# Optimization experiments

Measured on AMD Instinct MI355X. Metric: run time of the kernel, lower is better.

## Reference

```python
import jax, jax.numpy as jnp
import numpy as np

B, D, NF, L, G = 8192, 4096, 16, 32, 64  # batch, input_dim, num_factors, latent_per_factor, num groups
K = D // G  # group size (contiguous equal-size partition of columns)


def setup_inputs() -> dict:
    key = jax.random.key(0)
    k0, k1, k2, k3 = jax.random.split(key, 4)
    x = jax.random.normal(k0, (B, D), dtype=jnp.float32)
    # encoder: Linear(D,128) -> ReLU -> Linear(128, NF*L)
    W1 = jax.random.normal(k1, (D, 128), dtype=jnp.float32) * 0.02
    b1 = jnp.zeros((128,), dtype=jnp.float32)
    W2 = jax.random.normal(k2, (128, NF * L), dtype=jnp.float32) * 0.02
    b2 = jnp.zeros((NF * L,), dtype=jnp.float32)
    # k_matrix decoders: one [K, L] matrix per group, stacked -> [G, K, L]
    decoders = jax.random.normal(k3, (G, K, L), dtype=jnp.float32)
    return {"x": x, "W1": W1, "b1": b1, "W2": W2, "b2": b2, "decoders": decoders}


def reference(x, W1, b1, W2, b2, decoders):
    # encoder
    z = jax.nn.relu(x @ W1 + b1) @ W2 + b2                 # [B, NF*L]
    # reconstructions[:, group_g] = sum_j z_j @ D_g^T  ==  (sum_j z_j) @ D_g^T
    z_sum = z.reshape(x.shape[0], NF, L).sum(axis=1)        # [B, L]
    recon = jnp.einsum('bl,gkl->bgk', z_sum, decoders)      # [B, G, K]
    recon = recon.reshape(x.shape[0], G * K)                # [B, D] (contiguous groups)
    return (z, recon)
```

## Files before the change

### kernel.cpp

```cpp
#include <hip/hip_runtime.h>
#include <hip/hip_bf16.h>

#define BATCH 8192
#define DIN   4096
#define H1    128
#define NLAT  512
#define LAT   32
#define BM    16
#define BK    128
#define NSTEP (DIN / BK)
#define APITCH 136

typedef short bf16x8 __attribute__((ext_vector_type(8)));
typedef float f32x4  __attribute__((ext_vector_type(4)));

static __device__ __forceinline__ unsigned short f2bf(float f) {
  union { float f; unsigned u; } v; v.f = f;
  return (unsigned short)((v.u + 0x7FFFu + ((v.u >> 16) & 1u)) >> 16);
}

static __device__ __forceinline__ void cvtw8(unsigned short* p, f32x4 a, f32x4 b) {
  union { bf16x8 v; unsigned short u[8]; } o;
#pragma unroll
  for (int j = 0; j < 4; j++) { o.u[j] = f2bf(a[j]); o.u[4 + j] = f2bf(b[j]); }
  *(bf16x8*)p = o.v;
}

__global__ void prep_all(const float* __restrict__ W1, const float* __restrict__ W2,
                         const float* __restrict__ dec,
                         unsigned short* __restrict__ W1B,
                         unsigned short* __restrict__ W2B,
                         float* __restrict__ decT) {
  int b = blockIdx.x;
  int t = threadIdx.x;
  if (b < 256) {
    int gi = (b << 2) + (t >> 6);
    int lane = t & 63;
    int kb = ((gi >> 3) << 5) + ((lane >> 4) << 3);
    int c = ((gi & 7) << 4) + (lane & 15);
    union { bf16x8 v; unsigned short u[8]; } o;
#pragma unroll
    for (int j = 0; j < 8; j++) o.u[j] = f2bf(W1[(size_t)(kb + j) * H1 + c]);
    *(bf16x8*)(W1B + (((size_t)gi << 6) + (lane & 63)) * 8) = o.v;
  } else if (b < 288) {
    int gi = ((b - 256) << 2) + (t >> 6);
    int lane = t & 63;
    int kb = ((gi >> 5) << 5) + ((lane >> 4) << 3);
    int c = ((gi & 31) << 4) + (lane & 15);
    union { bf16x8 v; unsigned short u[8]; } o;
#pragma unroll
    for (int j = 0; j < 8; j++) o.u[j] = f2bf(W2[(size_t)(kb + j) * NLAT + c]);
    *(bf16x8*)(W2B + (((size_t)gi << 6) + lane) * 8) = o.v;
  } else {
    __shared__ float tbuf[32][33];
    int d0 = (b - 288) * 32;
    int tx = t & 31, ty = t >> 5;
#pragma unroll
    for (int i = 0; i < 32; i += 8)
      tbuf[ty + i][tx] = dec[(size_t)(d0 + ty + i) * LAT + tx];
    __syncthreads();
#pragma unroll
    for (int i = 0; i < 32; i += 8)
      decT[(size_t)(ty + i) * DIN + (d0 + tx)] = tbuf[tx][ty + i];
  }
}

__global__ __launch_bounds__(256, 4) void enc_kernel(
    const float* __restrict__ x, const unsigned short* __restrict__ W1B,
    const unsigned short* __restrict__ W2B,
    const float* __restrict__ b1, const float* __restrict__ b2,
    float* __restrict__ zout, float* __restrict__ zsumg) {
  __shared__ unsigned short As[2][BM * APITCH];
  __shared__ unsigned short hs[BM * APITCH];
  __shared__ float zsp[4][BM][33];

  const int t = threadIdx.x;
  const int rbase = blockIdx.x << 4;
  const int w = t >> 6, lane = t & 63;
  const int g = lane >> 4, fr = lane & 15;

  const int srow = t >> 4, skq = (t & 15) << 3;
  const float* xp = x + (size_t)(rbase + srow) * DIN + skq;
  const int wofs = srow * APITCH + skq;

  f32x4 acc[2];
  acc[0] = (f32x4){0.f, 0.f, 0.f, 0.f};
  acc[1] = (f32x4){0.f, 0.f, 0.f, 0.f};

  cvtw8(&As[0][wofs], *(const f32x4*)xp, *(const f32x4*)(xp + 4));
  __syncthreads();

  for (int s = 0; s < NSTEP; ++s) {
    f32x4 ra0, ra1;
    const bool more = (s + 1) < NSTEP;
    if (more) {
      ra0 = *(const f32x4*)(xp + (s + 1) * BK);
      ra1 = *(const f32x4*)(xp + (s + 1) * BK + 4);
    }
    const unsigned short* ab = &As[s & 1][0];
#pragma unroll
    for (int k32 = 0; k32 < 4; ++k32) {
      bf16x8 a0 = *(const bf16x8*)(ab + fr * APITCH + (((k32 << 2) + g) << 3));
#pragma unroll
      for (int cc = 0; cc < 2; ++cc) {
        bf16x8 bv = *(const bf16x8*)(W1B +
            ((((size_t)(((s << 2) + k32) << 3)) + (w << 1) + cc) << 9) + (lane << 3));
        acc[cc] = __builtin_amdgcn_mfma_f32_16x16x32_bf16(a0, bv, acc[cc], 0, 0, 0);
      }
    }
    if (more)
      cvtw8(&As[(s + 1) & 1][wofs], ra0, ra1);
    __syncthreads();
  }

  {
#pragma unroll
    for (int cc = 0; cc < 2; ++cc) {
      const int col = (w << 5) + (cc << 4) + fr;
      const float b1v = b1[col];
#pragma unroll
      for (int j = 0; j < 4; j++) {
        float h = fmaxf(acc[cc][j] + b1v, 0.f);
        hs[((g << 2) + j) * APITCH + col] = f2bf(h);
      }
    }
  }
  __syncthreads();

  f32x4 acc2[8];
#pragma unroll
  for (int i = 0; i < 8; i++) acc2[i] = (f32x4){0.f, 0.f, 0.f, 0.f};
#pragma unroll
  for (int k32 = 0; k32 < 4; ++k32) {
    bf16x8 a0 = *(const bf16x8*)(hs + fr * APITCH + (((k32 << 2) + g) << 3));
#pragma unroll
    for (int cc = 0; cc < 8; ++cc) {
      bf16x8 bv = *(const bf16x8*)(W2B +
          (((size_t)((k32 << 5) + (w << 3) + cc)) << 9) + (lane << 3));
      acc2[cc] = __builtin_amdgcn_mfma_f32_16x16x32_bf16(a0, bv, acc2[cc], 0, 0, 0);
    }
  }

  {
    f32x4 zv[8];
#pragma unroll
    for (int cc = 0; cc < 8; ++cc) {
      const float b2v = b2[(w << 7) + (cc << 4) + fr];
#pragma unroll
      for (int j = 0; j < 4; j++) zv[cc][j] = acc2[cc][j] + b2v;
    }
    const int row0 = g << 2;
#pragma unroll
    for (int j = 0; j < 4; j++) {
#pragma unroll
      for (int cc = 0; cc < 8; ++cc)
        zout[(size_t)(rbase + row0 + j) * NLAT + (w << 7) + (cc << 4) + fr] = zv[cc][j];
      zsp[w][row0 + j][fr]      = zv[0][j] + zv[2][j] + zv[4][j] + zv[6][j];
      zsp[w][row0 + j][16 + fr] = zv[1][j] + zv[3][j] + zv[5][j] + zv[7][j];
    }
  }
  __syncthreads();
#pragma unroll
  for (int i = 0; i < 2; i++) {
    int idx = t + (i << 8);
    int r = idx >> 5, l = idx & 31;
    float s = zsp[0][r][l] + zsp[1][r][l] + zsp[2][r][l] + zsp[3][r][l];
    zsumg[(size_t)(rbase + r) * LAT + l] = s;
  }
}

__global__ __launch_bounds__(256) void recon_kernel(
    const float* __restrict__ zsumg, const float* __restrict__ decT,
    float* __restrict__ rout) {
  __shared__ float zs[32][32];
  int t = threadIdx.x;
  int rbase = (blockIdx.x >> 4) << 5;
  int dcol0 = (blockIdx.x & 15) << 8;
  {
    int r = t >> 3, c4 = (t & 7) << 2;
    *(f32x4*)&zs[r][c4] = *(const f32x4*)(zsumg + (size_t)(rbase + r) * LAT + c4);
  }
  __syncthreads();
  int wq = t >> 6, lane = t & 63;
  int r0 = wq << 3;
  int dcol = dcol0 + (lane << 2);
  f32x4 acc[8];
#pragma unroll
  for (int r = 0; r < 8; r++) acc[r] = (f32x4){0.f, 0.f, 0.f, 0.f};
#pragma unroll 4
  for (int l = 0; l < 32; l++) {
    f32x4 dv = *(const f32x4*)(decT + (size_t)l * DIN + dcol);
#pragma unroll
    for (int r = 0; r < 8; r++) {
      float zv = zs[r0 + r][l];
#pragma unroll
      for (int j = 0; j < 4; j++) acc[r][j] += zv * dv[j];
    }
  }
#pragma unroll
  for (int r = 0; r < 8; r++)
    *(f32x4*)(rout + (size_t)(rbase + r0 + r) * DIN + dcol) = acc[r];
}

extern "C" void kernel_launch(void* const* d_in, const int* in_sizes, int n_in,
                              void* d_out, int out_size, void* d_ws, size_t ws_size,
                              hipStream_t stream) {
  const float* x   = (const float*)d_in[0];
  const float* W1  = (const float*)d_in[1];
  const float* b1  = (const float*)d_in[2];
  const float* W2  = (const float*)d_in[3];
  const float* b2  = (const float*)d_in[4];
  const float* dec = (const float*)d_in[5];
  float* zout = (float*)d_out;
  float* rout = zout + (size_t)BATCH * NLAT;

  char* ws = (char*)d_ws;
  unsigned short* W1B = (unsigned short*)ws;
  unsigned short* W2B = (unsigned short*)(ws + (1u << 20));
  float* decT  = (float*)(ws + (1u << 20) + (1u << 17));
  float* zsumg = (float*)(ws + (1u << 20) + (1u << 17) + (1u << 19));

  prep_all<<<dim3(416), 256, 0, stream>>>(W1, W2, dec, W1B, W2B, decT);
  enc_kernel<<<dim3(BATCH / BM), 256, 0, stream>>>(x, W1B, W2B, b1, b2, zout, zsumg);
  recon_kernel<<<dim3(4096), 256, 0, stream>>>(zsumg, decT, rout);
}
```

Before: 90.93 us.

## Split encoder K across warps with private LDS buffers and LDS reduction

The first encoder GEMM now splits the 4096-long K dimension into four slices, one per wavefront. Each wave streams its slice into a private double-buffered, XOR-swizzled LDS tile and computes all 128 hidden columns, so the block-wide barrier inside the K loop goes away. The four partial sums are then reduced through LDS, the bias and ReLU are applied, and the hidden layer is written to a swizzled bf16 tile for the second GEMM. In exchange the kernel uses more LDS and registers, launch bounds drop from 4 to 2 blocks per CU, and there is an extra reduction pass.

```diff
diff --git a/kernel.cpp b/kernel.cpp
--- a/kernel.cpp
+++ b/kernel.cpp
@@ -7,9 +7,9 @@
 #define NLAT  512
 #define LAT   32
 #define BM    16
-#define BK    128
-#define NSTEP (DIN / BK)
-#define APITCH 136
+#define BKW   64
+#define WSTEPS 16
+#define ABUF  1024
 
 typedef short bf16x8 __attribute__((ext_vector_type(8)));
 typedef float f32x4  __attribute__((ext_vector_type(4)));
@@ -41,7 +41,7 @@
     union { bf16x8 v; unsigned short u[8]; } o;
 #pragma unroll
     for (int j = 0; j < 8; j++) o.u[j] = f2bf(W1[(size_t)(kb + j) * H1 + c]);
-    *(bf16x8*)(W1B + (((size_t)gi << 6) + (lane & 63)) * 8) = o.v;
+    *(bf16x8*)(W1B + (((size_t)gi << 6) + lane) * 8) = o.v;
   } else if (b < 288) {
     int gi = ((b - 256) << 2) + (t >> 6);
     int lane = t & 63;
@@ -65,65 +65,94 @@
   }
 }
 
-__global__ __launch_bounds__(256, 4) void enc_kernel(
+__global__ __launch_bounds__(256, 2) void enc_kernel(
     const float* __restrict__ x, const unsigned short* __restrict__ W1B,
     const unsigned short* __restrict__ W2B,
     const float* __restrict__ b1, const float* __restrict__ b2,
     float* __restrict__ zout, float* __restrict__ zsumg) {
-  __shared__ unsigned short As[2][BM * APITCH];
-  __shared__ unsigned short hs[BM * APITCH];
-  __shared__ float zsp[4][BM][33];
+  __shared__ unsigned short Apriv[4 * 2 * ABUF];
+  __shared__ unsigned short hs[16 * 128];
+  __shared__ float pacc[4][16][132];
+  __shared__ float zsp[4][16][33];
 
   const int t = threadIdx.x;
   const int rbase = blockIdx.x << 4;
   const int w = t >> 6, lane = t & 63;
   const int g = lane >> 4, fr = lane & 15;
 
-  const int srow = t >> 4, skq = (t & 15) << 3;
-  const float* xp = x + (size_t)(rbase + srow) * DIN + skq;
-  const int wofs = srow * APITCH + skq;
-
-  f32x4 acc[2];
-  acc[0] = (f32x4){0.f, 0.f, 0.f, 0.f};
-  acc[1] = (f32x4){0.f, 0.f, 0.f, 0.f};
-
-  cvtw8(&As[0][wofs], *(const f32x4*)xp, *(const f32x4*)(xp + 4));
-  __syncthreads();
-
-  for (int s = 0; s < NSTEP; ++s) {
-    f32x4 ra0, ra1;
-    const bool more = (s + 1) < NSTEP;
+  const int srow = lane >> 2, sq = lane & 3;
+  const int k0 = w << 10;
+  const float* xp = x + (size_t)(rbase + srow) * DIN + k0 + (sq << 4);
+  unsigned short* abase = Apriv + (w << 11);
+  const int wg0 = ((sq << 1) ^ (srow & 7)) << 3;
+  const int wg1 = (((sq << 1) | 1) ^ (srow & 7)) << 3;
+  unsigned short* wrow = abase + srow * 64;
+
+  f32x4 acc[8];
+#pragma unroll
+  for (int i = 0; i < 8; i++) acc[i] = (f32x4){0.f, 0.f, 0.f, 0.f};
+
+  {
+    f32x4 q0 = *(const f32x4*)xp;
+    f32x4 q1 = *(const f32x4*)(xp + 4);
+    f32x4 q2 = *(const f32x4*)(xp + 8);
+    f32x4 q3 = *(const f32x4*)(xp + 12);
+    cvtw8(wrow + wg0, q0, q1);
+    cvtw8(wrow + wg1, q2, q3);
+  }
+
+  for (int s = 0; s < WSTEPS; ++s) {
+    f32x4 q0, q1, q2, q3;
+    const bool more = (s + 1) < WSTEPS;
     if (more) {
-      ra0 = *(const f32x4*)(xp + (s + 1) * BK);
-      ra1 = *(const f32x4*)(xp + (s + 1) * BK + 4);
-    }
-    const unsigned short* ab = &As[s & 1][0];
-#pragma unroll
-    for (int k32 = 0; k32 < 4; ++k32) {
-      bf16x8 a0 = *(const bf16x8*)(ab + fr * APITCH + (((k32 << 2) + g) << 3));
-#pragma unroll
-      for (int cc = 0; cc < 2; ++cc) {
-        bf16x8 bv = *(const bf16x8*)(W1B +
-            ((((size_t)(((s << 2) + k32) << 3)) + (w << 1) + cc) << 9) + (lane << 3));
-        acc[cc] = __builtin_amdgcn_mfma_f32_16x16x32_bf16(a0, bv, acc[cc], 0, 0, 0);
+      const float* np = xp + (s + 1) * BKW;
+      q0 = *(const f32x4*)np;
+      q1 = *(const f32x4*)(np + 4);
+      q2 = *(const f32x4*)(np + 8);
+      q3 = *(const f32x4*)(np + 12);
+    }
+    const unsigned short* ab = abase + (s & 1) * ABUF;
+    const int kbase = (w << 5) + (s << 1);
+#pragma unroll
+    for (int k32l = 0; k32l < 2; ++k32l) {
+      bf16x8 a = *(const bf16x8*)(ab + fr * 64 +
+                   ((((k32l << 2) + g) ^ (fr & 7)) << 3));
+      const unsigned short* bp = W1B + (((size_t)(kbase + k32l) << 3) << 9) + (lane << 3);
+#pragma unroll
+      for (int cf = 0; cf < 8; ++cf) {
+        bf16x8 bv = *(const bf16x8*)(bp + ((size_t)cf << 9));
+        acc[cf] = __builtin_amdgcn_mfma_f32_16x16x32_bf16(a, bv, acc[cf], 0, 0, 0);
       }
     }
-    if (more)
-      cvtw8(&As[(s + 1) & 1][wofs], ra0, ra1);
-    __syncthreads();
-  }
-
-  {
-#pragma unroll
-    for (int cc = 0; cc < 2; ++cc) {
-      const int col = (w << 5) + (cc << 4) + fr;
-      const float b1v = b1[col];
-#pragma unroll
-      for (int j = 0; j < 4; j++) {
-        float h = fmaxf(acc[cc][j] + b1v, 0.f);
-        hs[((g << 2) + j) * APITCH + col] = f2bf(h);
-      }
-    }
+    if (more) {
+      unsigned short* wr = abase + ((s + 1) & 1) * ABUF + srow * 64;
+      cvtw8(wr + wg0, q0, q1);
+      cvtw8(wr + wg1, q2, q3);
+    }
+  }
+
+#pragma unroll
+  for (int cf = 0; cf < 8; ++cf)
+#pragma unroll
+    for (int j = 0; j < 4; ++j)
+      pacc[w][(g << 2) + j][(cf << 4) + fr] = acc[cf][j];
+  __syncthreads();
+
+  {
+    const int r = t >> 4, c8 = (t & 15) << 3;
+    f32x4 s0, s1;
+#pragma unroll
+    for (int j = 0; j < 4; j++) { s0[j] = b1[c8 + j]; s1[j] = b1[c8 + 4 + j]; }
+#pragma unroll
+    for (int wv = 0; wv < 4; ++wv) {
+      f32x4 p0 = *(const f32x4*)&pacc[wv][r][c8];
+      f32x4 p1 = *(const f32x4*)&pacc[wv][r][c8 + 4];
+#pragma unroll
+      for (int j = 0; j < 4; j++) { s0[j] += p0[j]; s1[j] += p1[j]; }
+    }
+#pragma unroll
+    for (int j = 0; j < 4; j++) { s0[j] = fmaxf(s0[j], 0.f); s1[j] = fmaxf(s1[j], 0.f); }
+    cvtw8(hs + (r << 7) + (((t & 15) ^ (r & 15)) << 3), s0, s1);
   }
   __syncthreads();
 
@@ -132,7 +161,8 @@
   for (int i = 0; i < 8; i++) acc2[i] = (f32x4){0.f, 0.f, 0.f, 0.f};
 #pragma unroll
   for (int k32 = 0; k32 < 4; ++k32) {
-    bf16x8 a0 = *(const bf16x8*)(hs + fr * APITCH + (((k32 << 2) + g) << 3));
+    bf16x8 a0 = *(const bf16x8*)(hs + (fr << 7) +
+                  ((((k32 << 2) + g) ^ (fr & 15)) << 3));
 #pragma unroll
     for (int cc = 0; cc < 8; ++cc) {
       bf16x8 bv = *(const bf16x8*)(W2B +
```

Result: slower. 95.41 us (+4.9%).
